# Kernel optimization log

Hardware: AMD Instinct MI355X
Metric: run time of the kernel (lower is better)

## Reference

```python
import jax, jax.numpy as jnp
import numpy as np
import math

B, N, D, K = 4, 255, 256, 128
NODE_FEATURES_OFFSET = 128
MAX_Z = 101
NUM_EDGES = 2 * NODE_FEATURES_OFFSET + 1  # 257
NUM_DIR_KERNEL = 128  # FourierDirectionalEmbed num_kernel
ECFG_F = 20  # synthetic electron-config feature dim


def setup_inputs() -> dict:
    key = jax.random.key(0)
    ks = jax.random.split(key, 16)
    positions = jax.random.normal(ks[0], (B, N, 3), dtype=jnp.float32) * 3.0
    atomic_numbers = jax.random.randint(ks[1], (B, N), 1, MAX_Z, dtype=jnp.int32)
    s = 0.02
    emb_z = jax.random.normal(ks[2], (MAX_Z + 1, D), dtype=jnp.float32) * s
    electron_config = jax.random.uniform(ks[3], (MAX_Z + 1, ECFG_F), dtype=jnp.float32)
    config_W = jax.random.normal(ks[4], (ECFG_F, D), dtype=jnp.float32) * s
    config_b = jnp.zeros((D,), dtype=jnp.float32)
    mult_W = jax.random.normal(ks[5], (NODE_FEATURES_OFFSET, D), dtype=jnp.float32) * s
    charge_W = jax.random.normal(ks[6], (NODE_FEATURES_OFFSET, D), dtype=jnp.float32) * s
    gbf_means = jax.random.uniform(ks[7], (K,), dtype=jnp.float32, minval=0.0, maxval=7.0)
    gbf_stds = jax.random.uniform(ks[8], (K,), dtype=jnp.float32, minval=0.0, maxval=3.0)
    gbf_mul = jax.random.normal(ks[9], (NUM_EDGES,), dtype=jnp.float32).at[0].set(0.0)  # padding_idx=0
    gbf_bias = (jax.random.normal(ks[10], (NUM_EDGES,), dtype=jnp.float32) * 0.1).at[0].set(0.0)
    proj1_W = jax.random.normal(ks[11], (K, K), dtype=jnp.float32) * (1.0 / math.sqrt(K))
    proj1_b = jnp.zeros((K,), dtype=jnp.float32)
    proj2_W = jax.random.normal(ks[12], (K, D), dtype=jnp.float32) * (1.0 / math.sqrt(K))
    proj2_b = jnp.zeros((D,), dtype=jnp.float32)
    dir_W = jax.random.normal(ks[13], (2 * NUM_DIR_KERNEL, D), dtype=jnp.float32) * (1.0 / math.sqrt(2 * NUM_DIR_KERNEL))
    dir_b = jnp.zeros((D,), dtype=jnp.float32)
    return dict(positions=positions, atomic_numbers=atomic_numbers, emb_z=emb_z,
                electron_config=electron_config, config_W=config_W, config_b=config_b,
                mult_W=mult_W, charge_W=charge_W, gbf_means=gbf_means, gbf_stds=gbf_stds,
                gbf_mul=gbf_mul, gbf_bias=gbf_bias, proj1_W=proj1_W, proj1_b=proj1_b,
                proj2_W=proj2_W, proj2_b=proj2_b, dir_W=dir_W, dir_b=dir_b)


def _angular_freqs():
    min_angle = 1e-4
    half = NUM_DIR_KERNEL // 2
    wl_az = jnp.exp(jnp.linspace(math.log(2 * min_angle), math.log(2 * 2 * math.pi), half))
    wl_po = jnp.exp(jnp.linspace(math.log(2 * min_angle), math.log(2 * math.pi), half))
    return (2 * math.pi / wl_az).astype(jnp.float32), (2 * math.pi / wl_po).astype(jnp.float32)


def _forward(positions, atomic_numbers, emb_z, electron_config, config_W, config_b,
             mult_W, charge_W, gbf_means, gbf_stds, gbf_mul, gbf_bias,
             proj1_W, proj1_b, proj2_W, proj2_b, dir_W, dir_b):
    b = positions.shape[0]
    # add graph-level (CLS) token: zero position, z = MAX_Z = 101
    pos = jnp.concatenate([jnp.zeros_like(positions[:, :1]), positions], axis=1)  # [B,Np,3]
    z = jnp.concatenate([jnp.full_like(atomic_numbers[:, :1], MAX_Z), atomic_numbers], axis=1)  # [B,Np]
    npad = pos.shape[1]

    # --- node embedding: nuclear + electronic + multiplicity(1) + charge(0) ---
    elec = electron_config[z] @ config_W + config_b            # [B,Np,D]
    elec = elec.at[:, 0, :].set(0.0)                            # cls_token row zeroed
    node = emb_z[z] + elec + mult_W[1] + charge_W[0]           # [B,Np,D]

    # --- pairwise geometry: directions[b,i,j] = pos[j] - pos[i] ---
    d = pos[:, None, :, :] - pos[:, :, None, :]                # [B,Np,Np,3]
    sq = jnp.sum(d * d, axis=-1)
    dist = jnp.sqrt(sq + 1e-12)                                # [B,Np,Np]
    nd = d / (dist[..., None] + 1e-5)                          # normed directions, eps per source
    eye = jnp.eye(npad, dtype=bool)[None, :, :]
    x_safe = jnp.where(eye, 1.0, nd[..., 0])
    y_safe = jnp.where(eye, 0.0, nd[..., 1])
    azimuth = jnp.arctan2(y_safe, x_safe)                      # [B,Np,Np]
    polar = jnp.arccos(jnp.clip(nd[..., 2], -1.0 + 1e-6, 1.0 - 1e-6))

    # --- FourierDirectionalEmbed ---
    f_az, f_po = _angular_freqs()
    ph_az = azimuth[..., None] * f_az                          # [B,Np,Np,64]
    ph_po = polar[..., None] * f_po
    sinusoids = jnp.concatenate([jnp.sin(ph_az), jnp.cos(ph_az),
                                 jnp.sin(ph_po), jnp.cos(ph_po)], axis=-1)  # [B,Np,Np,256]
    dir_out = sinusoids @ dir_W + dir_b                        # [B,Np,Np,D]

    # --- Gaussian3DEmbed ---
    zi = z[:, :, None]
    zj = z[:, None, :] + NODE_FEATURES_OFFSET
    mul = gbf_mul[zi] + gbf_mul[zj]                            # sum over the 2 edge-type entries
    bias = gbf_bias[zi] + gbf_bias[zj]                         # [B,Np,Np]
    gx = (mul * dist + bias)[..., None]                        # [B,Np,Np,1] -> broadcast to K
    std = jnp.abs(gbf_stds) + 0.01
    pi_c = 3.14159
    gauss = jnp.exp(-0.5 * ((gx - gbf_means) / std) ** 2) / ((2 * pi_c) ** 0.5 * std)  # [B,Np,Np,K]
    h = jax.nn.gelu(gauss @ proj1_W + proj1_b, approximate=False)
    gbf_out = h @ proj2_W + proj2_b                            # [B,Np,Np,D]

    return node, gbf_out, dir_out


def reference(positions, atomic_numbers, emb_z, electron_config, config_W, config_b,
              mult_W, charge_W, gbf_means, gbf_stds, gbf_mul, gbf_bias,
              proj1_W, proj1_b, proj2_W, proj2_b, dir_W, dir_b):
    return _forward(positions, atomic_numbers, emb_z, electron_config, config_W, config_b,
                    mult_W, charge_W, gbf_means, gbf_stds, gbf_mul, gbf_bias,
                    proj1_W, proj1_b, proj2_W, proj2_b, dir_W, dir_b)
```

## Files before the change

kernel.cpp:

```cpp
#include <hip/hip_runtime.h>
#include <math.h>

typedef __bf16 bf16x8 __attribute__((ext_vector_type(8)));
typedef __bf16 bf16x4 __attribute__((ext_vector_type(4)));
typedef float f32x4 __attribute__((ext_vector_type(4)));

#define PI_D 3.14159265358979323846

__global__ void prep_kernel(const float* __restrict__ dir_W,
                            const float* __restrict__ proj1_W,
                            const float* __restrict__ proj2_W,
                            const float* __restrict__ gbf_stds,
                            __bf16* __restrict__ dirP, __bf16* __restrict__ p1P,
                            __bf16* __restrict__ p2P,
                            float* __restrict__ f_az, float* __restrict__ f_po,
                            float* __restrict__ inv_std, float* __restrict__ coef) {
  int tid = threadIdx.x + blockIdx.x * blockDim.x;
  int nth = gridDim.x * blockDim.x;
  for (int o = tid; o < 256 * 256; o += nth) {
    int j = o & 7, l = (o >> 3) & 63, ks = (o >> 9) & 7, nt = o >> 12;
    int d = nt * 16 + (l & 15);
    int s = ks * 32 + (l >> 4) * 8 + j;
    dirP[o] = (__bf16)dir_W[s * 256 + d];
  }
  for (int o = tid; o < 128 * 128; o += nth) {
    int j = o & 7, l = (o >> 3) & 63, ks = (o >> 9) & 3, nt = o >> 11;
    int ko = nt * 16 + (l & 15);
    int ki = ks * 32 + (l >> 4) * 8 + j;
    p1P[o] = (__bf16)proj1_W[ki * 128 + ko];
  }
  for (int o = tid; o < 128 * 256; o += nth) {
    int j = o & 7, l = (o >> 3) & 63, ks = (o >> 9) & 3, nt = o >> 11;
    int d = nt * 16 + (l & 15);
    int k = ks * 32 + (l >> 4) * 8 + j;
    p2P[o] = (__bf16)proj2_W[k * 256 + d];
  }
  if (blockIdx.x == 0 && threadIdx.x < 64) {
    int q = threadIdx.x;
    double l0 = log(2.0 * 1e-4);
    double l1a = log(2.0 * 2.0 * PI_D);
    double l1p = log(2.0 * PI_D);
    double ta = l0 + (l1a - l0) * (double)q / 63.0;
    double tp = l0 + (l1p - l0) * (double)q / 63.0;
    f_az[q] = (float)(2.0 * PI_D / exp(ta));
    f_po[q] = (float)(2.0 * PI_D / exp(tp));
  }
  if (blockIdx.x == 1 && threadIdx.x < 128) {
    int k = threadIdx.x;
    float sd = fabsf(gbf_stds[k]) + 0.01f;
    inv_std[k] = 1.0f / sd;
    coef[k] = (float)(1.0 / (sqrt(2.0 * 3.14159) * (double)sd));
  }
}

__global__ void node_kernel(const int* __restrict__ an, const float* __restrict__ emb_z,
                            const float* __restrict__ ec, const float* __restrict__ cW,
                            const float* __restrict__ cb, const float* __restrict__ mult_W,
                            const float* __restrict__ charge_W, float* __restrict__ out_node) {
  int bi = blockIdx.x;
  int b = bi >> 8, i = bi & 255;
  int d = threadIdx.x;
  int z = (i == 0) ? 101 : an[b * 255 + i - 1];
  float elec = 0.0f;
  if (i != 0) {
    for (int f = 0; f < 20; ++f) elec += ec[z * 20 + f] * cW[f * 256 + d];
    elec += cb[d];
  }
  float v = emb_z[z * 256 + d] + elec + mult_W[256 + d] + charge_W[d];
  __builtin_nontemporal_store(v, &out_node[(size_t)bi * 256 + d]);
}

__global__ __launch_bounds__(256, 4) void pair_kernel(
    const float* __restrict__ positions, const int* __restrict__ atomic_numbers,
    const float* __restrict__ gbf_means, const float* __restrict__ gbf_mul,
    const float* __restrict__ gbf_bias, const float* __restrict__ proj1_b,
    const float* __restrict__ proj2_b, const float* __restrict__ dir_b,
    const __bf16* __restrict__ dirP, const __bf16* __restrict__ p1P,
    const __bf16* __restrict__ p2P, const float* __restrict__ f_az,
    const float* __restrict__ f_po, const float* __restrict__ inv_stdv,
    const float* __restrict__ coefv, float* __restrict__ out_gbf,
    float* __restrict__ out_dir) {
  __shared__ __align__(16) __bf16 buf[64 * 136];
  __shared__ float s_az[64], s_po[64], s_gx[64];

  const int tid = threadIdx.x;
  const int bid = blockIdx.x;
  const int jt = bid & 3;
  const int i = (bid >> 2) & 255;
  const int b = bid >> 10;
  const int j0 = jt * 64;
  const long pairbase = ((long)(b * 256 + i)) * 256 + j0;

  const int lane = tid & 63, wv = tid >> 6;
  const int lr = lane & 15, kb = lane >> 4;

  if (tid < 64) {
    int p = tid, j = j0 + p;
    float pxi = 0.f, pyi = 0.f, pzi = 0.f, pxj = 0.f, pyj = 0.f, pzj = 0.f;
    if (i != 0) { const float* q = positions + ((size_t)b * 255 + (i - 1)) * 3; pxi = q[0]; pyi = q[1]; pzi = q[2]; }
    if (j != 0) { const float* q = positions + ((size_t)b * 255 + (j - 1)) * 3; pxj = q[0]; pyj = q[1]; pzj = q[2]; }
    float dx = pxj - pxi, dy = pyj - pyi, dz = pzj - pzi;
    float sq = dx * dx + dy * dy + dz * dz;
    float dist = sqrtf(sq + 1e-12f);
    float inv = 1.0f / (dist + 1e-5f);
    float ndx = dx * inv, ndy = dy * inv, ndz = dz * inv;
    bool diag = (i == j);
    float xs = diag ? 1.0f : ndx;
    float ys = diag ? 0.0f : ndy;
    s_az[p] = atan2f(ys, xs);
    float cz = fminf(fmaxf(ndz, -1.0f + 1e-6f), 1.0f - 1e-6f);
    s_po[p] = acosf(cz);
    int zi = (i == 0) ? 101 : atomic_numbers[b * 255 + i - 1];
    int zj = ((j == 0) ? 101 : atomic_numbers[b * 255 + j - 1]) + 128;
    float mul = gbf_mul[zi] + gbf_mul[zj];
    float bia = gbf_bias[zi] + gbf_bias[zj];
    s_gx[p] = mul * dist + bia;
  }
  __syncthreads();

  f32x4 acc[4][4];
#pragma unroll
  for (int mtl = 0; mtl < 4; ++mtl)
#pragma unroll
    for (int np = 0; np < 4; ++np) acc[mtl][np] = (f32x4){0.f, 0.f, 0.f, 0.f};

  for (int half = 0; half < 2; ++half) {
#pragma unroll
    for (int it = 0; it < 2; ++it) {
      int job = tid + it * 256;
      int p = job >> 3, g = job & 7;
      int q0 = g * 8;
      float ang = half ? s_po[p] : s_az[p];
      const float* ft = half ? f_po : f_az;
      bf16x8 sv, cv;
#pragma unroll
      for (int t = 0; t < 8; ++t) {
        float ph = ang * ft[q0 + t];
        double r = (double)ph * 0.15915494309189535;
        double fr = r - rint(r);
        float frf = (float)fr;
        sv[t] = (__bf16)__builtin_amdgcn_sinf(frf);
        cv[t] = (__bf16)__builtin_amdgcn_cosf(frf);
      }
      *(bf16x8*)(buf + p * 136 + q0) = sv;
      *(bf16x8*)(buf + p * 136 + 64 + q0) = cv;
    }
    __syncthreads();
#pragma unroll
    for (int ksl = 0; ksl < 4; ++ksl) {
      int ks = half * 4 + ksl;
      bf16x8 bfr[4];
#pragma unroll
      for (int np = 0; np < 4; ++np)
        bfr[np] = *(const bf16x8*)(buf + (np * 16 + lr) * 136 + ksl * 32 + kb * 8);
#pragma unroll
      for (int mtl = 0; mtl < 4; ++mtl) {
        int mtile = mtl * 4 + wv;
        bf16x8 af = *(const bf16x8*)(dirP + (((size_t)mtile * 8 + ks) * 64 + lane) * 8);
#pragma unroll
        for (int np = 0; np < 4; ++np)
          acc[mtl][np] = __builtin_amdgcn_mfma_f32_16x16x32_bf16(af, bfr[np], acc[mtl][np], 0, 0, 0);
      }
    }
    __syncthreads();
  }

#pragma unroll
  for (int mtl = 0; mtl < 4; ++mtl) {
    int dcol0 = (mtl * 4 + wv) * 16 + kb * 4;
    f32x4 bias = *(const f32x4*)(dir_b + dcol0);
#pragma unroll
    for (int np = 0; np < 4; ++np) {
      f32x4 v = acc[mtl][np] + bias;
      __builtin_nontemporal_store(v, (f32x4*)(out_dir + (pairbase + np * 16 + lr) * 256 + dcol0));
    }
  }

#pragma unroll
  for (int it = 0; it < 4; ++it) {
    int job = tid + it * 256;
    int p = job >> 4, g = job & 15;
    int k0 = g * 8;
    float gx = s_gx[p];
    bf16x8 gv;
#pragma unroll
    for (int t = 0; t < 8; ++t) {
      int k = k0 + t;
      float x = (gx - gbf_means[k]) * inv_stdv[k];
      gv[t] = (__bf16)(exp2f(-0.72134752044448170f * x * x) * coefv[k]);
    }
    *(bf16x8*)(buf + p * 136 + k0) = gv;
  }
  __syncthreads();

  f32x4 acc1[2][4];
#pragma unroll
  for (int mtl = 0; mtl < 2; ++mtl)
#pragma unroll
    for (int np = 0; np < 4; ++np) acc1[mtl][np] = (f32x4){0.f, 0.f, 0.f, 0.f};
#pragma unroll
  for (int ksl = 0; ksl < 4; ++ksl) {
    bf16x8 bfr[4];
#pragma unroll
    for (int np = 0; np < 4; ++np)
      bfr[np] = *(const bf16x8*)(buf + (np * 16 + lr) * 136 + ksl * 32 + kb * 8);
#pragma unroll
    for (int mtl = 0; mtl < 2; ++mtl) {
      int mtile = mtl * 4 + wv;
      bf16x8 af = *(const bf16x8*)(p1P + (((size_t)mtile * 4 + ksl) * 64 + lane) * 8);
#pragma unroll
      for (int np = 0; np < 4; ++np)
        acc1[mtl][np] = __builtin_amdgcn_mfma_f32_16x16x32_bf16(af, bfr[np], acc1[mtl][np], 0, 0, 0);
    }
  }
  __syncthreads();

#pragma unroll
  for (int mtl = 0; mtl < 2; ++mtl) {
    int ko0 = (mtl * 4 + wv) * 16 + kb * 4;
    f32x4 pb = *(const f32x4*)(proj1_b + ko0);
#pragma unroll
    for (int np = 0; np < 4; ++np) {
      f32x4 hv = acc1[mtl][np] + pb;
      bf16x4 hb;
#pragma unroll
      for (int r = 0; r < 4; ++r) {
        float v = hv[r];
        v = 0.5f * v * (1.0f + erff(v * 0.70710678118654752f));
        hb[r] = (__bf16)v;
      }
      *(bf16x4*)(buf + (np * 16 + lr) * 136 + ko0) = hb;
    }
  }
  __syncthreads();

  f32x4 acc2[4][4];
#pragma unroll
  for (int mtl = 0; mtl < 4; ++mtl)
#pragma unroll
    for (int np = 0; np < 4; ++np) acc2[mtl][np] = (f32x4){0.f, 0.f, 0.f, 0.f};
#pragma unroll
  for (int ksl = 0; ksl < 4; ++ksl) {
    bf16x8 bfr[4];
#pragma unroll
    for (int np = 0; np < 4; ++np)
      bfr[np] = *(const bf16x8*)(buf + (np * 16 + lr) * 136 + ksl * 32 + kb * 8);
#pragma unroll
    for (int mtl = 0; mtl < 4; ++mtl) {
      int mtile = mtl * 4 + wv;
      bf16x8 af = *(const bf16x8*)(p2P + (((size_t)mtile * 4 + ksl) * 64 + lane) * 8);
#pragma unroll
      for (int np = 0; np < 4; ++np)
        acc2[mtl][np] = __builtin_amdgcn_mfma_f32_16x16x32_bf16(af, bfr[np], acc2[mtl][np], 0, 0, 0);
    }
  }
#pragma unroll
  for (int mtl = 0; mtl < 4; ++mtl) {
    int dcol0 = (mtl * 4 + wv) * 16 + kb * 4;
    f32x4 bias = *(const f32x4*)(proj2_b + dcol0);
#pragma unroll
    for (int np = 0; np < 4; ++np) {
      f32x4 v = acc2[mtl][np] + bias;
      __builtin_nontemporal_store(v, (f32x4*)(out_gbf + (pairbase + np * 16 + lr) * 256 + dcol0));
    }
  }
}

extern "C" void kernel_launch(void* const* d_in, const int* in_sizes, int n_in,
                              void* d_out, int out_size, void* d_ws, size_t ws_size,
                              hipStream_t stream) {
  const float* positions = (const float*)d_in[0];
  const int* atomic_numbers = (const int*)d_in[1];
  const float* emb_z = (const float*)d_in[2];
  const float* electron_config = (const float*)d_in[3];
  const float* config_W = (const float*)d_in[4];
  const float* config_b = (const float*)d_in[5];
  const float* mult_W = (const float*)d_in[6];
  const float* charge_W = (const float*)d_in[7];
  const float* gbf_means = (const float*)d_in[8];
  const float* gbf_stds = (const float*)d_in[9];
  const float* gbf_mul = (const float*)d_in[10];
  const float* gbf_bias = (const float*)d_in[11];
  const float* proj1_W = (const float*)d_in[12];
  const float* proj1_b = (const float*)d_in[13];
  const float* proj2_W = (const float*)d_in[14];
  const float* proj2_b = (const float*)d_in[15];
  const float* dir_W = (const float*)d_in[16];
  const float* dir_b = (const float*)d_in[17];

  float* out = (float*)d_out;
  float* out_node = out;
  float* out_gbf = out + 262144;
  float* out_dir = out + 262144 + 67108864;

  char* ws = (char*)d_ws;
  __bf16* dirP = (__bf16*)(ws);
  __bf16* p1P = (__bf16*)(ws + 131072);
  __bf16* p2P = (__bf16*)(ws + 131072 + 32768);
  float* f_az = (float*)(ws + 229376);
  float* f_po = (float*)(ws + 229376 + 256);
  float* inv_std = (float*)(ws + 229376 + 512);
  float* coef = (float*)(ws + 229376 + 1024);

  prep_kernel<<<64, 256, 0, stream>>>(dir_W, proj1_W, proj2_W, gbf_stds, dirP, p1P,
                                      p2P, f_az, f_po, inv_std, coef);
  node_kernel<<<1024, 256, 0, stream>>>(atomic_numbers, emb_z, electron_config,
                                        config_W, config_b, mult_W, charge_W, out_node);
  pair_kernel<<<4096, 256, 0, stream>>>(positions, atomic_numbers, gbf_means, gbf_mul,
                                        gbf_bias, proj1_b, proj2_b, dir_b, dirP, p1P,
                                        p2P, f_az, f_po, inv_std, coef, out_gbf, out_dir);
}
```

Baseline: 160.7 us.

## Replace double-precision range reduction, fold Gaussian constants, lighten barriers, vectorize prep

The sin/cos phase range reduction now uses a float split-constant (hi/lo 1/2π) instead of double math. The Gaussian affine terms are precomputed into per-k (A, B) pairs so each element costs one FMA and an exp2. Frequency and Gaussian constants are hoisted into registers per thread. __syncthreads is replaced by an LDS-only waitcnt plus s_barrier, and the prep kernel writes packed bf16x8 vectors. The float reduction may lose accuracy for large phases, and the barrier change relies on only LDS traffic needing ordering.

```diff
diff --git a/kernel.cpp b/kernel.cpp
--- a/kernel.cpp
+++ b/kernel.cpp
@@ -4,36 +4,56 @@
 typedef __bf16 bf16x8 __attribute__((ext_vector_type(8)));
 typedef __bf16 bf16x4 __attribute__((ext_vector_type(4)));
 typedef float f32x4 __attribute__((ext_vector_type(4)));
+typedef float f32x2 __attribute__((ext_vector_type(2)));
 
 #define PI_D 3.14159265358979323846
+#define IH 0.15915494f
+#define IL 6.4206383e-9f
+
+__device__ __forceinline__ void bar_lds() {
+  __builtin_amdgcn_sched_barrier(0);
+  asm volatile("s_waitcnt lgkmcnt(0)" ::: "memory");
+  __builtin_amdgcn_s_barrier();
+  __builtin_amdgcn_sched_barrier(0);
+}
 
 __global__ void prep_kernel(const float* __restrict__ dir_W,
                             const float* __restrict__ proj1_W,
                             const float* __restrict__ proj2_W,
                             const float* __restrict__ gbf_stds,
+                            const float* __restrict__ gbf_means,
                             __bf16* __restrict__ dirP, __bf16* __restrict__ p1P,
                             __bf16* __restrict__ p2P,
                             float* __restrict__ f_az, float* __restrict__ f_po,
-                            float* __restrict__ inv_std, float* __restrict__ coef) {
+                            f32x2* __restrict__ gAB, float* __restrict__ gcoef) {
   int tid = threadIdx.x + blockIdx.x * blockDim.x;
   int nth = gridDim.x * blockDim.x;
-  for (int o = tid; o < 256 * 256; o += nth) {
-    int j = o & 7, l = (o >> 3) & 63, ks = (o >> 9) & 7, nt = o >> 12;
+  for (int o8 = tid; o8 < 8192; o8 += nth) {
+    int l = o8 & 63, ks = (o8 >> 6) & 7, nt = o8 >> 9;
     int d = nt * 16 + (l & 15);
-    int s = ks * 32 + (l >> 4) * 8 + j;
-    dirP[o] = (__bf16)dir_W[s * 256 + d];
-  }
-  for (int o = tid; o < 128 * 128; o += nth) {
-    int j = o & 7, l = (o >> 3) & 63, ks = (o >> 9) & 3, nt = o >> 11;
+    int s0 = ks * 32 + (l >> 4) * 8;
+    bf16x8 v;
+#pragma unroll
+    for (int j = 0; j < 8; ++j) v[j] = (__bf16)dir_W[(s0 + j) * 256 + d];
+    *(bf16x8*)(dirP + o8 * 8) = v;
+  }
+  for (int o8 = tid; o8 < 2048; o8 += nth) {
+    int l = o8 & 63, ks = (o8 >> 6) & 3, nt = o8 >> 8;
     int ko = nt * 16 + (l & 15);
-    int ki = ks * 32 + (l >> 4) * 8 + j;
-    p1P[o] = (__bf16)proj1_W[ki * 128 + ko];
-  }
-  for (int o = tid; o < 128 * 256; o += nth) {
-    int j = o & 7, l = (o >> 3) & 63, ks = (o >> 9) & 3, nt = o >> 11;
+    int k0 = ks * 32 + (l >> 4) * 8;
+    bf16x8 v;
+#pragma unroll
+    for (int j = 0; j < 8; ++j) v[j] = (__bf16)proj1_W[(k0 + j) * 128 + ko];
+    *(bf16x8*)(p1P + o8 * 8) = v;
+  }
+  for (int o8 = tid; o8 < 4096; o8 += nth) {
+    int l = o8 & 63, ks = (o8 >> 6) & 3, nt = o8 >> 8;
     int d = nt * 16 + (l & 15);
-    int k = ks * 32 + (l >> 4) * 8 + j;
-    p2P[o] = (__bf16)proj2_W[k * 256 + d];
+    int k0 = ks * 32 + (l >> 4) * 8;
+    bf16x8 v;
+#pragma unroll
+    for (int j = 0; j < 8; ++j) v[j] = (__bf16)proj2_W[(k0 + j) * 256 + d];
+    *(bf16x8*)(p2P + o8 * 8) = v;
   }
   if (blockIdx.x == 0 && threadIdx.x < 64) {
     int q = threadIdx.x;
@@ -47,9 +67,14 @@
   }
   if (blockIdx.x == 1 && threadIdx.x < 128) {
     int k = threadIdx.x;
-    float sd = fabsf(gbf_stds[k]) + 0.01f;
-    inv_std[k] = 1.0f / sd;
-    coef[k] = (float)(1.0 / (sqrt(2.0 * 3.14159) * (double)sd));
+    double sd = (double)(fabsf(gbf_stds[k]) + 0.01f);
+    double c = sqrt(0.7213475204444817);
+    double A = c / sd;
+    f32x2 ab;
+    ab.x = (float)A;
+    ab.y = (float)(-A * (double)gbf_means[k]);
+    gAB[k] = ab;
+    gcoef[k] = (float)(1.0 / (sqrt(2.0 * 3.14159) * sd));
   }
 }
 
@@ -72,14 +97,13 @@
 
 __global__ __launch_bounds__(256, 4) void pair_kernel(
     const float* __restrict__ positions, const int* __restrict__ atomic_numbers,
-    const float* __restrict__ gbf_means, const float* __restrict__ gbf_mul,
-    const float* __restrict__ gbf_bias, const float* __restrict__ proj1_b,
-    const float* __restrict__ proj2_b, const float* __restrict__ dir_b,
-    const __bf16* __restrict__ dirP, const __bf16* __restrict__ p1P,
-    const __bf16* __restrict__ p2P, const float* __restrict__ f_az,
-    const float* __restrict__ f_po, const float* __restrict__ inv_stdv,
-    const float* __restrict__ coefv, float* __restrict__ out_gbf,
-    float* __restrict__ out_dir) {
+    const float* __restrict__ gbf_mul, const float* __restrict__ gbf_bias,
+    const float* __restrict__ proj1_b, const float* __restrict__ proj2_b,
+    const float* __restrict__ dir_b, const __bf16* __restrict__ dirP,
+    const __bf16* __restrict__ p1P, const __bf16* __restrict__ p2P,
+    const float* __restrict__ f_az, const float* __restrict__ f_po,
+    const f32x2* __restrict__ gAB, const float* __restrict__ gcoef,
+    float* __restrict__ out_gbf, float* __restrict__ out_dir) {
   __shared__ __align__(16) __bf16 buf[64 * 136];
   __shared__ float s_az[64], s_po[64], s_gx[64];
 
@@ -93,6 +117,11 @@
 
   const int lane = tid & 63, wv = tid >> 6;
   const int lr = lane & 15, kb = lane >> 4;
+
+  const int q8 = (tid & 7) * 8;
+  const int pr2 = tid >> 3;
+  const int k0g = (tid & 15) * 8;
+  const int prow = tid >> 4;
 
   if (tid < 64) {
     int p = tid, j = j0 + p;
@@ -116,7 +145,7 @@
     float bia = gbf_bias[zi] + gbf_bias[zj];
     s_gx[p] = mul * dist + bia;
   }
-  __syncthreads();
+  bar_lds();
 
   f32x4 acc[4][4];
 #pragma unroll
@@ -125,27 +154,27 @@
     for (int np = 0; np < 4; ++np) acc[mtl][np] = (f32x4){0.f, 0.f, 0.f, 0.f};
 
   for (int half = 0; half < 2; ++half) {
+    const float* ft = half ? f_po : f_az;
+    float fv[8];
+#pragma unroll
+    for (int t = 0; t < 8; ++t) fv[t] = ft[q8 + t];
 #pragma unroll
     for (int it = 0; it < 2; ++it) {
-      int job = tid + it * 256;
-      int p = job >> 3, g = job & 7;
-      int q0 = g * 8;
+      int p = pr2 + it * 32;
       float ang = half ? s_po[p] : s_az[p];
-      const float* ft = half ? f_po : f_az;
       bf16x8 sv, cv;
 #pragma unroll
       for (int t = 0; t < 8; ++t) {
-        float ph = ang * ft[q0 + t];
-        double r = (double)ph * 0.15915494309189535;
-        double fr = r - rint(r);
-        float frf = (float)fr;
-        sv[t] = (__bf16)__builtin_amdgcn_sinf(frf);
-        cv[t] = (__bf16)__builtin_amdgcn_cosf(frf);
+        float ph = ang * fv[t];
+        float n = __builtin_rintf(ph * IH);
+        float fr = __builtin_fmaf(ph, IH, -n) + ph * IL;
+        sv[t] = (__bf16)__builtin_amdgcn_sinf(fr);
+        cv[t] = (__bf16)__builtin_amdgcn_cosf(fr);
       }
-      *(bf16x8*)(buf + p * 136 + q0) = sv;
-      *(bf16x8*)(buf + p * 136 + 64 + q0) = cv;
-    }
-    __syncthreads();
+      *(bf16x8*)(buf + p * 136 + q8) = sv;
+      *(bf16x8*)(buf + p * 136 + 64 + q8) = cv;
+    }
+    bar_lds();
 #pragma unroll
     for (int ksl = 0; ksl < 4; ++ksl) {
       int ks = half * 4 + ksl;
@@ -162,8 +191,13 @@
           acc[mtl][np] = __builtin_amdgcn_mfma_f32_16x16x32_bf16(af, bfr[np], acc[mtl][np], 0, 0, 0);
       }
     }
-    __syncthreads();
-  }
+    bar_lds();
+  }
+
+  f32x2 abv[8];
+  float gcv[8];
+#pragma unroll
+  for (int t = 0; t < 8; ++t) { abv[t] = gAB[k0g + t]; gcv[t] = gcoef[k0g + t]; }
 
 #pragma unroll
   for (int mtl = 0; mtl < 4; ++mtl) {
@@ -178,20 +212,17 @@
 
 #pragma unroll
   for (int it = 0; it < 4; ++it) {
-    int job = tid + it * 256;
-    int p = job >> 4, g = job & 15;
-    int k0 = g * 8;
+    int p = prow + it * 16;
     float gx = s_gx[p];
     bf16x8 gv;
 #pragma unroll
     for (int t = 0; t < 8; ++t) {
-      int k = k0 + t;
-      float x = (gx - gbf_means[k]) * inv_stdv[k];
-      gv[t] = (__bf16)(exp2f(-0.72134752044448170f * x * x) * coefv[k]);
-    }
-    *(bf16x8*)(buf + p * 136 + k0) = gv;
-  }
-  __syncthreads();
+      float y = __builtin_fmaf(gx, abv[t].x, abv[t].y);
+      gv[t] = (__bf16)(exp2f(-y * y) * gcv[t]);
+    }
+    *(bf16x8*)(buf + p * 136 + k0g) = gv;
+  }
+  bar_lds();
 
   f32x4 acc1[2][4];
 #pragma unroll
@@ -213,7 +244,7 @@
         acc1[mtl][np] = __builtin_amdgcn_mfma_f32_16x16x32_bf16(af, bfr[np], acc1[mtl][np], 0, 0, 0);
     }
   }
-  __syncthreads();
+  bar_lds();
 
 #pragma unroll
   for (int mtl = 0; mtl < 2; ++mtl) {
@@ -232,7 +263,7 @@
       *(bf16x4*)(buf + (np * 16 + lr) * 136 + ko0) = hb;
     }
   }
-  __syncthreads();
+  bar_lds();
 
   f32x4 acc2[4][4];
 #pragma unroll
@@ -296,17 +327,17 @@
   char* ws = (char*)d_ws;
   __bf16* dirP = (__bf16*)(ws);
   __bf16* p1P = (__bf16*)(ws + 131072);
-  __bf16* p2P = (__bf16*)(ws + 131072 + 32768);
+  __bf16* p2P = (__bf16*)(ws + 163840);
   float* f_az = (float*)(ws + 229376);
   float* f_po = (float*)(ws + 229376 + 256);
-  float* inv_std = (float*)(ws + 229376 + 512);
-  float* coef = (float*)(ws + 229376 + 1024);
-
-  prep_kernel<<<64, 256, 0, stream>>>(dir_W, proj1_W, proj2_W, gbf_stds, dirP, p1P,
-                                      p2P, f_az, f_po, inv_std, coef);
+  f32x2* gAB = (f32x2*)(ws + 229376 + 512);
+  float* gcoef = (float*)(ws + 229376 + 1536);
+
+  prep_kernel<<<64, 256, 0, stream>>>(dir_W, proj1_W, proj2_W, gbf_stds, gbf_means,
+                                      dirP, p1P, p2P, f_az, f_po, gAB, gcoef);
   node_kernel<<<1024, 256, 0, stream>>>(atomic_numbers, emb_z, electron_config,
                                         config_W, config_b, mult_W, charge_W, out_node);
-  pair_kernel<<<4096, 256, 0, stream>>>(positions, atomic_numbers, gbf_means, gbf_mul,
-                                        gbf_bias, proj1_b, proj2_b, dir_b, dirP, p1P,
-                                        p2P, f_az, f_po, inv_std, coef, out_gbf, out_dir);
-}
+  pair_kernel<<<4096, 256, 0, stream>>>(positions, atomic_numbers, gbf_mul, gbf_bias,
+                                        proj1_b, proj2_b, dir_b, dirP, p1P, p2P,
+                                        f_az, f_po, gAB, gcoef, out_gbf, out_dir);
+}
```

Result: no change. 157.8 us (-1.8%).
